# Kernel tuning notes

Measured on AMD Instinct MI355X. Metric: run time of the kernel, lower is better.

Reference implementation:

```python
import jax, jax.numpy as jnp
import numpy as np

N_NODES = 50000
N_EDGES = 800000
IN_DIM = 128
HID = 32
HEADS = 4
OUT_DIM = 64
NEG_SLOPE = 0.2


def _glorot(key, shape):
    fan = shape[0] + shape[-1] if len(shape) > 1 else shape[-1]
    lim = jnp.sqrt(6.0 / fan)
    return jax.random.uniform(key, shape, jnp.float32, -lim, lim)


def setup_inputs() -> dict:
    key = jax.random.key(0)
    ks = jax.random.split(key, 10)
    x = jax.random.normal(ks[0], (N_NODES, IN_DIM), jnp.float32)
    edge_index = jax.random.randint(ks[1], (2, N_EDGES), 0, N_NODES, jnp.int32)
    # layer 1: in=IN_DIM, heads=HEADS, out=HID, concat
    W1 = _glorot(ks[2], (IN_DIM, HEADS * HID))
    a_src1 = _glorot(ks[3], (HEADS, HID))
    a_dst1 = _glorot(ks[4], (HEADS, HID))
    b1 = jnp.zeros((HEADS * HID,), jnp.float32)
    # layer 2: in=HEADS*HID, heads=1, out=OUT_DIM, mean
    W2 = _glorot(ks[5], (HEADS * HID, OUT_DIM))
    a_src2 = _glorot(ks[6], (1, OUT_DIM))
    a_dst2 = _glorot(ks[7], (1, OUT_DIM))
    b2 = jnp.zeros((OUT_DIM,), jnp.float32)
    return {"x": x, "edge_index": edge_index, "W1": W1, "a_src1": a_src1,
            "a_dst1": a_dst1, "b1": b1, "W2": W2, "a_src2": a_src2,
            "a_dst2": a_dst2, "b2": b2}


def gat_conv(x, src, dst, W, a_src, a_dst, bias, heads, out_ch, concat, num_nodes):
    # x: [N, in]; src/dst: [E] (self-loops already included)
    h = (x @ W).reshape(num_nodes, heads, out_ch)          # [N, H, F]
    alpha_s = jnp.einsum('nhf,hf->nh', h, a_src)           # [N, H]
    alpha_d = jnp.einsum('nhf,hf->nh', h, a_dst)
    e = alpha_s[src] + alpha_d[dst]                        # [E, H]
    e = jnp.where(e >= 0, e, NEG_SLOPE * e)                # leaky relu
    # segment softmax over destination neighborhoods
    e_max = jax.ops.segment_max(e, dst, num_segments=num_nodes)
    ex = jnp.exp(e - e_max[dst])
    denom = jax.ops.segment_sum(ex, dst, num_segments=num_nodes)
    alpha = ex / (denom[dst] + 1e-16)                      # [E, H]
    msg = h[src] * alpha[:, :, None]                       # [E, H, F]
    out = jax.ops.segment_sum(msg, dst, num_segments=num_nodes)  # [N, H, F]
    if concat:
        out = out.reshape(num_nodes, heads * out_ch)
    else:
        out = out.mean(axis=1)
    return out + bias


def reference(x, edge_index, W1, a_src1, a_dst1, b1, W2, a_src2, a_dst2, b2):
    n = x.shape[0]
    # PyG GATConv default add_self_loops=True
    loop = jnp.arange(n, dtype=edge_index.dtype)
    src = jnp.concatenate([edge_index[0], loop])
    dst = jnp.concatenate([edge_index[1], loop])
    h = gat_conv(x, src, dst, W1, a_src1, a_dst1, b1, HEADS, HID, True, n)
    h = jax.nn.relu(h)
    out = gat_conv(h, src, dst, W2, a_src2, a_dst2, b2, 1, OUT_DIM, False, n)
    return out
```

## Files before the change

### kernel.cpp

```cpp
#include <hip/hip_runtime.h>
#include <hip/hip_fp16.h>
#include <math.h>


#define NEG_SLOPE 0.2f
#define CAP 80

__device__ __forceinline__ float lrelu_exp(float e) {
    e = (e >= 0.f) ? e : NEG_SLOPE * e;
    return __expf(e);
}

__global__ __launch_bounds__(256) void build_kernel(
    const float* __restrict__ x, const float* __restrict__ W1,
    const float* __restrict__ a_src1, const float* __restrict__ a_dst1,
    __half* __restrict__ h1h, float* __restrict__ as1, float* __restrict__ ad1,
    const int* __restrict__ src, const int* __restrict__ dst,
    int* __restrict__ deg, unsigned short* __restrict__ col,
    int N, int E, int Gg) {
    __shared__ float Ws[32 * 128];
    __shared__ float xs[64 * 32];
    const int tid = threadIdx.x;

    if (blockIdx.x >= Gg) {
        const int base = (blockIdx.x - Gg) * 2048 + tid * 8;
        int s[8], d[8];
        if (base + 8 <= E) {
            int4 a0 = *(const int4*)&src[base];
            int4 a1 = *(const int4*)&src[base + 4];
            int4 c0 = *(const int4*)&dst[base];
            int4 c1 = *(const int4*)&dst[base + 4];
            s[0]=a0.x; s[1]=a0.y; s[2]=a0.z; s[3]=a0.w;
            s[4]=a1.x; s[5]=a1.y; s[6]=a1.z; s[7]=a1.w;
            d[0]=c0.x; d[1]=c0.y; d[2]=c0.z; d[3]=c0.w;
            d[4]=c1.x; d[5]=c1.y; d[6]=c1.z; d[7]=c1.w;
        } else {
#pragma unroll
            for (int u = 0; u < 8; ++u) {
                int i = base + u;
                if (i < E) { s[u] = src[i]; d[u] = dst[i]; }
                else       { s[u] = -1;     d[u] = -1; }
            }
        }
        int p[8];
#pragma unroll
        for (int u = 0; u < 8; ++u)
            if (d[u] >= 0) p[u] = atomicAdd(&deg[d[u]], 1);
#pragma unroll
        for (int u = 0; u < 8; ++u)
            if (d[u] >= 0 && p[u] < CAP)
                col[d[u] * CAP + p[u]] = (unsigned short)s[u];
        return;
    }

    const int tf = tid & 31;
    const int tn = tid >> 5;
    const int nb = blockIdx.x * 64;
    float acc[8][4];
#pragma unroll
    for (int i = 0; i < 8; ++i)
#pragma unroll
        for (int j = 0; j < 4; ++j) acc[i][j] = 0.f;

    for (int kc = 0; kc < 128; kc += 32) {
#pragma unroll
        for (int l = 0; l < 4; ++l) {
            int idx = tid + l * 256;
            int k = idx >> 5, f4 = idx & 31;
            *(float4*)&Ws[k * 128 + f4 * 4] =
                *(const float4*)&W1[(kc + k) * 128 + f4 * 4];
        }
#pragma unroll
        for (int l = 0; l < 2; ++l) {
            int idx = tid + l * 256;
            int n = idx >> 3, j = idx & 7;
            int gn = nb + n; if (gn >= N) gn = N - 1;
            *(float4*)&xs[n * 32 + j * 4] =
                *(const float4*)&x[gn * 128 + kc + j * 4];
        }
        __syncthreads();
#pragma unroll
        for (int k = 0; k < 32; ++k) {
            float4 w = *(const float4*)&Ws[k * 128 + tf * 4];
#pragma unroll
            for (int i = 0; i < 8; ++i) {
                float xv = xs[(tn * 8 + i) * 32 + k];
                acc[i][0] += xv * w.x; acc[i][1] += xv * w.y;
                acc[i][2] += xv * w.z; acc[i][3] += xv * w.w;
            }
        }
        __syncthreads();
    }
    float4 asv = *(const float4*)&a_src1[tf * 4];
    float4 adv = *(const float4*)&a_dst1[tf * 4];
    const int head = tf >> 3;
    const int lane8 = tf & 7;
#pragma unroll
    for (int i = 0; i < 8; ++i) {
        int n = nb + tn * 8 + i;
        if (n < N) {
            __half2 p0 = __floats2half2_rn(acc[i][0], acc[i][1]);
            __half2 p1 = __floats2half2_rn(acc[i][2], acc[i][3]);
            uint2 pk;
            pk.x = *(unsigned*)&p0;
            pk.y = *(unsigned*)&p1;
            *(uint2*)&h1h[(size_t)n * 128 + tf * 4] = pk;
        }
        float s = acc[i][0]*asv.x + acc[i][1]*asv.y + acc[i][2]*asv.z + acc[i][3]*asv.w;
        float d = acc[i][0]*adv.x + acc[i][1]*adv.y + acc[i][2]*adv.z + acc[i][3]*adv.w;
        s += __shfl_down(s, 4); d += __shfl_down(d, 4);
        s += __shfl_down(s, 2); d += __shfl_down(d, 2);
        s += __shfl_down(s, 1); d += __shfl_down(d, 1);
        if (lane8 == 0 && n < N) { as1[n * 4 + head] = s; ad1[n * 4 + head] = d; }
    }
}

__global__ __launch_bounds__(256) void agg1mm_kernel(
    const __half2* __restrict__ h1h2, const float* __restrict__ as1,
    const float* __restrict__ ad1, const float* __restrict__ b1,
    const float* __restrict__ W2, const float* __restrict__ a_src2,
    const float* __restrict__ a_dst2, const int* __restrict__ deg,
    const unsigned short* __restrict__ col,
    __half* __restrict__ h2h, float* __restrict__ as2, float* __restrict__ ad2,
    int N) {
    __shared__ float hrs[4][128];
    __shared__ float part[16][64];
    const int tid = threadIdx.x;
    const int w = tid >> 6;
    const int lane = tid & 63;
    const int d = blockIdx.x * 4 + w;

    if (d < N) {
        const int hsel = lane >> 4;
        const float adh = ad1[4 * d + hsel];
        const int dg = min(deg[d], CAP);
        const int beg = d * CAP;

        float wself = lrelu_exp(as1[4 * d + hsel] + adh);
        float2 vself = __half22float2(h1h2[(size_t)d * 64 + lane]);
        float den = wself, accx = wself * vself.x, accy = wself * vself.y;

        for (int c = 0; c < dg; c += 64) {
            const int m = min(64, dg - c);
            int scol = 0;
            if (lane < m) scol = (int)col[beg + c + lane];
            int jj = 0;
            for (; jj + 8 <= m; jj += 8) {
                int ss[8]; float av[8]; __half2 v[8];
#pragma unroll
                for (int u = 0; u < 8; ++u) ss[u] = __shfl(scol, jj + u, 64);
#pragma unroll
                for (int u = 0; u < 8; ++u) av[u] = as1[4 * ss[u] + hsel];
#pragma unroll
                for (int u = 0; u < 8; ++u) v[u] = h1h2[(size_t)ss[u] * 64 + lane];
#pragma unroll
                for (int u = 0; u < 8; ++u) {
                    float wt = lrelu_exp(av[u] + adh);
                    float2 vf = __half22float2(v[u]);
                    den += wt;
                    accx += wt * vf.x;
                    accy += wt * vf.y;
                }
            }
            for (; jj < m; ++jj) {
                int s = __shfl(scol, jj, 64);
                float wt = lrelu_exp(as1[4 * s + hsel] + adh);
                float2 vf = __half22float2(h1h2[(size_t)s * 64 + lane]);
                den += wt;
                accx += wt * vf.x;
                accy += wt * vf.y;
            }
        }
        const float inv = 1.f / (den + 1e-16f);
        float2 bv = *(const float2*)&b1[lane * 2];
        float2 o;
        o.x = fmaxf(accx * inv + bv.x, 0.f);
        o.y = fmaxf(accy * inv + bv.y, 0.f);
        *(float2*)&hrs[w][lane * 2] = o;
    } else {
        hrs[w][lane * 2] = 0.f;
        hrs[w][lane * 2 + 1] = 0.f;
    }
    __syncthreads();

    float p0 = 0.f, p1 = 0.f, p2 = 0.f, p3 = 0.f;
#pragma unroll
    for (int kk = 0; kk < 32; ++kk) {
        const int k = w * 32 + kk;
        const float wv = W2[k * 64 + lane];
        p0 += hrs[0][k] * wv;
        p1 += hrs[1][k] * wv;
        p2 += hrs[2][k] * wv;
        p3 += hrs[3][k] * wv;
    }
    part[w * 4 + 0][lane] = p0;
    part[w * 4 + 1][lane] = p1;
    part[w * 4 + 2][lane] = p2;
    part[w * 4 + 3][lane] = p3;
    __syncthreads();

    if (d < N) {
        float h2f = part[0 * 4 + w][lane] + part[1 * 4 + w][lane] +
                    part[2 * 4 + w][lane] + part[3 * 4 + w][lane];
        h2h[(size_t)d * 64 + lane] = __float2half(h2f);
        float s = h2f * a_src2[lane];
        float dv = h2f * a_dst2[lane];
        s += __shfl_down(s, 32); dv += __shfl_down(dv, 32);
        s += __shfl_down(s, 16); dv += __shfl_down(dv, 16);
        s += __shfl_down(s, 8);  dv += __shfl_down(dv, 8);
        s += __shfl_down(s, 4);  dv += __shfl_down(dv, 4);
        s += __shfl_down(s, 2);  dv += __shfl_down(dv, 2);
        s += __shfl_down(s, 1);  dv += __shfl_down(dv, 1);
        if (lane == 0) { as2[d] = s; ad2[d] = dv; }
    }
}

__global__ __launch_bounds__(256) void agg2_kernel(
    const __half* __restrict__ h2h, const float* __restrict__ as2,
    const float* __restrict__ ad2, const float* __restrict__ b2,
    const int* __restrict__ deg, const unsigned short* __restrict__ col,
    float* __restrict__ out, int N) {
    const int lane = threadIdx.x & 63;
    const int d = blockIdx.x * 4 + (threadIdx.x >> 6);
    if (d >= N) return;
    const int dg = min(deg[d], CAP);
    const int beg = d * CAP;
    const float adv = ad2[d];

    float wself = lrelu_exp(as2[d] + adv);
    float den = wself;
    float acc = wself * __half2float(h2h[(size_t)d * 64 + lane]);

    for (int c = 0; c < dg; c += 64) {
        const int m = min(64, dg - c);
        int scol = 0; float wreg = 0.f;
        if (lane < m) {
            scol = (int)col[beg + c + lane];
            wreg = lrelu_exp(as2[scol] + adv);
        }
        int jj = 0;
        for (; jj + 8 <= m; jj += 8) {
            int ss[8]; float wv[8]; __half v[8];
#pragma unroll
            for (int u = 0; u < 8; ++u) {
                ss[u] = __shfl(scol, jj + u, 64);
                wv[u] = __shfl(wreg, jj + u, 64);
            }
#pragma unroll
            for (int u = 0; u < 8; ++u) v[u] = h2h[(size_t)ss[u] * 64 + lane];
#pragma unroll
            for (int u = 0; u < 8; ++u) {
                den += wv[u];
                acc += wv[u] * __half2float(v[u]);
            }
        }
        for (; jj < m; ++jj) {
            int s = __shfl(scol, jj, 64);
            float wt = __shfl(wreg, jj, 64);
            den += wt;
            acc += wt * __half2float(h2h[(size_t)s * 64 + lane]);
        }
    }
    out[(size_t)d * 64 + lane] = acc / (den + 1e-16f) + b2[lane];
}

extern "C" void kernel_launch(void* const* d_in, const int* in_sizes, int n_in,
                              void* d_out, int out_size, void* d_ws, size_t ws_size,
                              hipStream_t stream) {
    const float* x      = (const float*)d_in[0];
    const int*   eidx   = (const int*)d_in[1];
    const float* W1     = (const float*)d_in[2];
    const float* a_src1 = (const float*)d_in[3];
    const float* a_dst1 = (const float*)d_in[4];
    const float* b1     = (const float*)d_in[5];
    const float* W2     = (const float*)d_in[6];
    const float* a_src2 = (const float*)d_in[7];
    const float* a_dst2 = (const float*)d_in[8];
    const float* b2     = (const float*)d_in[9];
    float* out = (float*)d_out;

    const int N = in_sizes[0] / 128;
    const int E = in_sizes[1] / 2;

    const int* src = eidx;
    const int* dst = eidx + E;

    float* ws_f = (float*)d_ws;
    float* as1 = ws_f;
    float* ad1 = as1 + (size_t)N * 4;
    float* as2 = ad1 + (size_t)N * 4;
    float* ad2 = as2 + (size_t)N;
    __half* h1h = (__half*)(ad2 + (size_t)N);
    __half* h2h = h1h + (size_t)N * 128;
    int* deg = (int*)(h2h + (size_t)N * 64);
    unsigned short* col = (unsigned short*)(deg + N);

    const int Gg = (N + 63) / 64;
    const int Gs = (E + 2047) / 2048;

    hipMemsetAsync(deg, 0, (size_t)N * sizeof(int), stream);

    build_kernel<<<Gg + Gs, 256, 0, stream>>>(x, W1, a_src1, a_dst1,
                                              h1h, as1, ad1,
                                              src, dst, deg, col, N, E, Gg);

    agg1mm_kernel<<<(N + 3) / 4, 256, 0, stream>>>(
        (const __half2*)h1h, as1, ad1, b1, W2, a_src2, a_dst2,
        deg, col, h2h, as2, ad2, N);

    agg2_kernel<<<(N + 3) / 4, 256, 0, stream>>>(h2h, as2, ad2, b2,
                                                 deg, col, out, N);
}
```

Measured before the change: 211.9 us.

## Partition CSR build by destination range and use scalar column loads in aggregation

```diff
diff --git a/kernel.cpp b/kernel.cpp
--- a/kernel.cpp
+++ b/kernel.cpp
@@ -23,7 +23,11 @@
     const int tid = threadIdx.x;
 
     if (blockIdx.x >= Gg) {
-        const int base = (blockIdx.x - Gg) * 2048 + tid * 8;
+        const int part = blockIdx.x & 7;
+        const int stripe = (blockIdx.x - Gg) >> 3;
+        const int psz = (N + 7) / 8;
+        const int dlo = part * psz;
+        const int base = stripe * 2048 + tid * 8;
         int s[8], d[8];
         if (base + 8 <= E) {
             int4 a0 = *(const int4*)&src[base];
@@ -39,17 +43,16 @@
             for (int u = 0; u < 8; ++u) {
                 int i = base + u;
                 if (i < E) { s[u] = src[i]; d[u] = dst[i]; }
-                else       { s[u] = -1;     d[u] = -1; }
-            }
-        }
-        int p[8];
-#pragma unroll
-        for (int u = 0; u < 8; ++u)
-            if (d[u] >= 0) p[u] = atomicAdd(&deg[d[u]], 1);
-#pragma unroll
-        for (int u = 0; u < 8; ++u)
-            if (d[u] >= 0 && p[u] < CAP)
-                col[d[u] * CAP + p[u]] = (unsigned short)s[u];
+                else       { s[u] = -1;     d[u] = -(1 << 30); }
+            }
+        }
+#pragma unroll
+        for (int u = 0; u < 8; ++u) {
+            if ((unsigned)(d[u] - dlo) < (unsigned)psz && d[u] < N) {
+                int p = atomicAdd(&deg[d[u]], 1);
+                if (p < CAP) col[d[u] * CAP + p] = (unsigned short)s[u];
+            }
+        }
         return;
     }
 
@@ -115,7 +118,7 @@
     }
 }
 
-__global__ __launch_bounds__(256) void agg1mm_kernel(
+__global__ __launch_bounds__(128) void agg1mm_kernel(
     const __half2* __restrict__ h1h2, const float* __restrict__ as1,
     const float* __restrict__ ad1, const float* __restrict__ b1,
     const float* __restrict__ W2, const float* __restrict__ a_src2,
@@ -123,53 +126,59 @@
     const unsigned short* __restrict__ col,
     __half* __restrict__ h2h, float* __restrict__ as2, float* __restrict__ ad2,
     int N) {
-    __shared__ float hrs[4][128];
-    __shared__ float part[16][64];
+    __shared__ float hrs[2][128];
+    __shared__ float part[2][2][64];
     const int tid = threadIdx.x;
     const int w = tid >> 6;
     const int lane = tid & 63;
-    const int d = blockIdx.x * 4 + w;
+    const int d = blockIdx.x * 2 + w;
 
     if (d < N) {
         const int hsel = lane >> 4;
         const float adh = ad1[4 * d + hsel];
-        const int dg = min(deg[d], CAP);
-        const int beg = d * CAP;
+        int dg = min(deg[d], CAP);
+        dg = __builtin_amdgcn_readfirstlane(dg);
+        const int beg = __builtin_amdgcn_readfirstlane(d * CAP);
 
         float wself = lrelu_exp(as1[4 * d + hsel] + adh);
         float2 vself = __half22float2(h1h2[(size_t)d * 64 + lane]);
         float den = wself, accx = wself * vself.x, accy = wself * vself.y;
 
-        for (int c = 0; c < dg; c += 64) {
-            const int m = min(64, dg - c);
-            int scol = 0;
-            if (lane < m) scol = (int)col[beg + c + lane];
-            int jj = 0;
-            for (; jj + 8 <= m; jj += 8) {
-                int ss[8]; float av[8]; __half2 v[8];
-#pragma unroll
-                for (int u = 0; u < 8; ++u) ss[u] = __shfl(scol, jj + u, 64);
-#pragma unroll
-                for (int u = 0; u < 8; ++u) av[u] = as1[4 * ss[u] + hsel];
-#pragma unroll
-                for (int u = 0; u < 8; ++u) v[u] = h1h2[(size_t)ss[u] * 64 + lane];
-#pragma unroll
-                for (int u = 0; u < 8; ++u) {
-                    float wt = lrelu_exp(av[u] + adh);
-                    float2 vf = __half22float2(v[u]);
-                    den += wt;
-                    accx += wt * vf.x;
-                    accy += wt * vf.y;
-                }
-            }
-            for (; jj < m; ++jj) {
-                int s = __shfl(scol, jj, 64);
-                float wt = lrelu_exp(as1[4 * s + hsel] + adh);
-                float2 vf = __half22float2(h1h2[(size_t)s * 64 + lane]);
+        int jj = 0;
+        for (; jj + 8 <= dg; jj += 8) {
+            uint4 cw = *(const uint4*)&col[beg + jj];
+            int ss[8];
+            ss[0] = cw.x & 0xffff; ss[1] = cw.x >> 16;
+            ss[2] = cw.y & 0xffff; ss[3] = cw.y >> 16;
+            ss[4] = cw.z & 0xffff; ss[5] = cw.z >> 16;
+            ss[6] = cw.w & 0xffff; ss[7] = cw.w >> 16;
+            __half2 v[8]; float av[8];
+#pragma unroll
+            for (int u = 0; u < 8; ++u) {
+                const __half2* rp = h1h2 + (size_t)ss[u] * 64;
+                v[u] = rp[lane];
+            }
+#pragma unroll
+            for (int u = 0; u < 8; ++u) {
+                const float* ap = as1 + 4 * ss[u];
+                av[u] = ap[hsel];
+            }
+#pragma unroll
+            for (int u = 0; u < 8; ++u) {
+                float wt = lrelu_exp(av[u] + adh);
+                float2 vf = __half22float2(v[u]);
                 den += wt;
                 accx += wt * vf.x;
                 accy += wt * vf.y;
             }
+        }
+        for (; jj < dg; ++jj) {
+            int s = (int)col[beg + jj];
+            float wt = lrelu_exp(as1[4 * s + hsel] + adh);
+            float2 vf = __half22float2(h1h2[(size_t)s * 64 + lane]);
+            den += wt;
+            accx += wt * vf.x;
+            accy += wt * vf.y;
         }
         const float inv = 1.f / (den + 1e-16f);
         float2 bv = *(const float2*)&b1[lane * 2];
@@ -183,25 +192,20 @@
     }
     __syncthreads();
 
-    float p0 = 0.f, p1 = 0.f, p2 = 0.f, p3 = 0.f;
-#pragma unroll
-    for (int kk = 0; kk < 32; ++kk) {
-        const int k = w * 32 + kk;
+    float p0 = 0.f, p1 = 0.f;
+#pragma unroll
+    for (int kk = 0; kk < 64; ++kk) {
+        const int k = w * 64 + kk;
         const float wv = W2[k * 64 + lane];
         p0 += hrs[0][k] * wv;
         p1 += hrs[1][k] * wv;
-        p2 += hrs[2][k] * wv;
-        p3 += hrs[3][k] * wv;
-    }
-    part[w * 4 + 0][lane] = p0;
-    part[w * 4 + 1][lane] = p1;
-    part[w * 4 + 2][lane] = p2;
-    part[w * 4 + 3][lane] = p3;
+    }
+    part[w][0][lane] = p0;
+    part[w][1][lane] = p1;
     __syncthreads();
 
     if (d < N) {
-        float h2f = part[0 * 4 + w][lane] + part[1 * 4 + w][lane] +
-                    part[2 * 4 + w][lane] + part[3 * 4 + w][lane];
+        float h2f = part[0][w][lane] + part[1][w][lane];
         h2h[(size_t)d * 64 + lane] = __float2half(h2f);
         float s = h2f * a_src2[lane];
         float dv = h2f * a_dst2[lane];
@@ -223,43 +227,43 @@
     const int lane = threadIdx.x & 63;
     const int d = blockIdx.x * 4 + (threadIdx.x >> 6);
     if (d >= N) return;
-    const int dg = min(deg[d], CAP);
-    const int beg = d * CAP;
+    int dg = min(deg[d], CAP);
+    dg = __builtin_amdgcn_readfirstlane(dg);
+    const int beg = __builtin_amdgcn_readfirstlane(d * CAP);
     const float adv = ad2[d];
 
     float wself = lrelu_exp(as2[d] + adv);
     float den = wself;
     float acc = wself * __half2float(h2h[(size_t)d * 64 + lane]);
 
-    for (int c = 0; c < dg; c += 64) {
-        const int m = min(64, dg - c);
-        int scol = 0; float wreg = 0.f;
-        if (lane < m) {
-            scol = (int)col[beg + c + lane];
-            wreg = lrelu_exp(as2[scol] + adv);
-        }
-        int jj = 0;
-        for (; jj + 8 <= m; jj += 8) {
-            int ss[8]; float wv[8]; __half v[8];
-#pragma unroll
-            for (int u = 0; u < 8; ++u) {
-                ss[u] = __shfl(scol, jj + u, 64);
-                wv[u] = __shfl(wreg, jj + u, 64);
-            }
-#pragma unroll
-            for (int u = 0; u < 8; ++u) v[u] = h2h[(size_t)ss[u] * 64 + lane];
-#pragma unroll
-            for (int u = 0; u < 8; ++u) {
-                den += wv[u];
-                acc += wv[u] * __half2float(v[u]);
-            }
-        }
-        for (; jj < m; ++jj) {
-            int s = __shfl(scol, jj, 64);
-            float wt = __shfl(wreg, jj, 64);
+    int jj = 0;
+    for (; jj + 8 <= dg; jj += 8) {
+        uint4 cw = *(const uint4*)&col[beg + jj];
+        int ss[8];
+        ss[0] = cw.x & 0xffff; ss[1] = cw.x >> 16;
+        ss[2] = cw.y & 0xffff; ss[3] = cw.y >> 16;
+        ss[4] = cw.z & 0xffff; ss[5] = cw.z >> 16;
+        ss[6] = cw.w & 0xffff; ss[7] = cw.w >> 16;
+        __half v[8]; float av[8];
+#pragma unroll
+        for (int u = 0; u < 8; ++u) {
+            const __half* rp = h2h + (size_t)ss[u] * 64;
+            v[u] = rp[lane];
+        }
+#pragma unroll
+        for (int u = 0; u < 8; ++u) av[u] = as2[ss[u]];
+#pragma unroll
+        for (int u = 0; u < 8; ++u) {
+            float wt = lrelu_exp(av[u] + adv);
             den += wt;
-            acc += wt * __half2float(h2h[(size_t)s * 64 + lane]);
-        }
+            acc += wt * __half2float(v[u]);
+        }
+    }
+    for (; jj < dg; ++jj) {
+        int s = (int)col[beg + jj];
+        float wt = lrelu_exp(as2[s] + adv);
+        den += wt;
+        acc += wt * __half2float(h2h[(size_t)s * 64 + lane]);
     }
     out[(size_t)d * 64 + lane] = acc / (den + 1e-16f) + b2[lane];
 }
@@ -296,7 +300,7 @@
     unsigned short* col = (unsigned short*)(deg + N);
 
     const int Gg = (N + 63) / 64;
-    const int Gs = (E + 2047) / 2048;
+    const int Gs = ((E + 2047) / 2048) * 8;
 
     hipMemsetAsync(deg, 0, (size_t)N * sizeof(int), stream);
 
@@ -304,7 +308,7 @@
                                               h1h, as1, ad1,
                                               src, dst, deg, col, N, E, Gg);
 
-    agg1mm_kernel<<<(N + 3) / 4, 256, 0, stream>>>(
+    agg1mm_kernel<<<(N + 1) / 2, 128, 0, stream>>>(
         (const __half2*)h1h, as1, ad1, b1, W2, a_src2, a_dst2,
         deg, col, h2h, as2, ad2, N);
 
```

Measured after the change: 232.4 us. +9.7%, slower.
